# Optimization experiments

Measured on AMD Instinct MI355X. Metric: run time of the kernel, lower is better.

Reference implementation:

```python
import jax, jax.numpy as jnp
import numpy as np

EMBED_DIM = 1024
HEADS = 16
HEAD_DIM = EMBED_DIM // HEADS


def setup_inputs() -> dict:
    key = jax.random.key(0)
    ks = jax.random.split(key, 5)
    B, N, C = 2, 2048, EMBED_DIM
    scale = 1.0 / np.sqrt(C)
    x = jax.random.normal(ks[0], (B, N, C), dtype=jnp.float32)
    W_qkv = jax.random.normal(ks[1], (C, 3 * C), dtype=jnp.float32) * scale
    b_qkv = jax.random.normal(ks[2], (3 * C,), dtype=jnp.float32) * 0.01
    W_out = jax.random.normal(ks[3], (C, C), dtype=jnp.float32) * scale
    b_out = jax.random.normal(ks[4], (C,), dtype=jnp.float32) * 0.01
    return {"x": x, "W_qkv": W_qkv, "b_qkv": b_qkv, "W_out": W_out, "b_out": b_out}


def reference(x, W_qkv, b_qkv, W_out, b_out):
    B, N, C = x.shape
    qkv = x @ W_qkv + b_qkv                      # [B, N, 3C]
    qkv = qkv.reshape(B, N, 3, HEADS, HEAD_DIM)
    qkv = jnp.transpose(qkv, (2, 0, 3, 1, 4))    # [3, B, H, N, d]
    q, k, v = qkv[0], qkv[1], qkv[2]
    attn = jnp.einsum('bhnd,bhmd->bhnm', q, k) / np.sqrt(HEAD_DIM)
    attn = jax.nn.softmax(attn, axis=-1)
    out = jnp.einsum('bhnm,bhmd->bhnd', attn, v)  # [B, H, N, d]
    out = jnp.transpose(out, (0, 2, 1, 3)).reshape(B, N, C)
    return out @ W_out + b_out
```

## Files before the change

kernel.cpp:

```cpp
#include <hip/hip_runtime.h>
#include <stdint.h>

typedef __bf16 bf16_t;
typedef bf16_t bf16x8 __attribute__((ext_vector_type(8)));
typedef bf16_t bf16x2v __attribute__((ext_vector_type(2)));
typedef short short4v __attribute__((ext_vector_type(4)));
typedef float f32x4 __attribute__((ext_vector_type(4)));
typedef uint32_t u32x2 __attribute__((ext_vector_type(2)));

#define BATCH 2
#define SEQ 2048
#define CDIM 1024
#define NH 16
#define HD 64

#define QSCALE 0.18033688011f

__device__ __forceinline__ uint16_t f32_bf16(float f) {
    __bf16 h = (__bf16)f;
    return __builtin_bit_cast(uint16_t, h);
}

__device__ __forceinline__ uint32_t pack_bf16(float a, float b) {
    bf16x2v t;
    t.x = (__bf16)a;
    t.y = (__bf16)b;
    return __builtin_bit_cast(uint32_t, t);
}

__device__ __forceinline__ bf16x8 ld8(const uint16_t* p) {
    return *reinterpret_cast<const bf16x8*>(p);
}

__device__ __forceinline__ void gld16(const uint16_t* g, uint16_t* l) {
    __builtin_amdgcn_global_load_lds(
        (__attribute__((address_space(1))) void*)(g),
        (__attribute__((address_space(3))) void*)(l), 16, 0, 0);
}

#define LDS_FENCE() asm volatile("s_waitcnt lgkmcnt(0)" ::: "memory")

__global__ __launch_bounds__(256) void cast_f32_bf16(
        const float* __restrict__ in, uint16_t* __restrict__ out, int n) {
    int i = (blockIdx.x * 256 + threadIdx.x) * 4;
    if (i < n) {
        float4 v = *(const float4*)(in + i);
        ushort4 o;
        o.x = f32_bf16(v.x);
        o.y = f32_bf16(v.y);
        o.z = f32_bf16(v.z);
        o.w = f32_bf16(v.w);
        *(ushort4*)(out + i) = o;
    }
}

__global__ __launch_bounds__(256) void transpose_cast(
        const float* __restrict__ in, uint16_t* __restrict__ out, int R, int Cc) {
    __shared__ float tile[32][33];
    int c0 = blockIdx.x * 32, r0 = blockIdx.y * 32;
    int tx = threadIdx.x, ty = threadIdx.y;
#pragma unroll
    for (int i = 0; i < 4; i++) {
        int r = ty + i * 8;
        tile[r][tx] = in[(size_t)(r0 + r) * Cc + c0 + tx];
    }
    __syncthreads();
#pragma unroll
    for (int i = 0; i < 4; i++) {
        int rr = ty + i * 8;
        out[(size_t)(c0 + rr) * R + r0 + tx] = f32_bf16(tile[tx][rr]);
    }
}

__global__ __launch_bounds__(256) void gemm128(
        const uint16_t* __restrict__ A, const uint16_t* __restrict__ Bt, int K,
        const float* __restrict__ bias, int mode,
        uint16_t* __restrict__ qw, uint16_t* __restrict__ kw, uint16_t* __restrict__ vt,
        float* __restrict__ out) {
    __shared__ uint16_t As[128 * 32];
    __shared__ uint16_t Bs[128 * 32];
    __shared__ uint16_t Ts[4][64 * 68];
    const int m0 = blockIdx.y * 128, n0 = blockIdx.x * 128;
    const int tid = threadIdx.x;
    const int w = tid >> 6, lane = tid & 63;
    const int quad = lane >> 4, l16 = lane & 15;
    const int wm = (w >> 1) * 64, wn = (w & 1) * 64;

    const int srow = lane >> 2;
    const int schunk = (lane & 3) ^ (srow & 3);
    const int seg0 = w * 2, seg1 = seg0 + 1;
    const uint16_t* a0 = A + (size_t)(m0 + seg0 * 16 + srow) * K + schunk * 8;
    const uint16_t* a1 = A + (size_t)(m0 + seg1 * 16 + srow) * K + schunk * 8;
    const uint16_t* b0 = Bt + (size_t)(n0 + seg0 * 16 + srow) * K + schunk * 8;
    const uint16_t* b1 = Bt + (size_t)(n0 + seg1 * 16 + srow) * K + schunk * 8;
    uint16_t* la0 = &As[seg0 * 512];
    uint16_t* la1 = &As[seg1 * 512];
    uint16_t* lb0 = &Bs[seg0 * 512];
    uint16_t* lb1 = &Bs[seg1 * 512];

    const int cslot = (quad ^ (l16 & 3)) * 8;

    f32x4 acc[4][4] = {};

    for (int k0 = 0; k0 < K; k0 += 32) {
        gld16(a0 + k0, la0);
        gld16(a1 + k0, la1);
        gld16(b0 + k0, lb0);
        gld16(b1 + k0, lb1);
        __syncthreads();
        bf16x8 af[4], bfr[4];
#pragma unroll
        for (int i = 0; i < 4; i++) af[i] = ld8(&As[(wm + i * 16 + l16) * 32 + cslot]);
#pragma unroll
        for (int i = 0; i < 4; i++) bfr[i] = ld8(&Bs[(wn + i * 16 + l16) * 32 + cslot]);
#pragma unroll
        for (int i = 0; i < 4; i++)
#pragma unroll
            for (int j = 0; j < 4; j++)
                acc[i][j] = __builtin_amdgcn_mfma_f32_16x16x32_bf16(af[i], bfr[j], acc[i][j], 0, 0, 0);
        __syncthreads();
    }

    const int nbase = n0 + wn;
    float bj[4];
#pragma unroll
    for (int j = 0; j < 4; j++) bj[j] = bias[nbase + j * 16 + l16];

    if (mode == 1) {
#pragma unroll
        for (int j = 0; j < 4; j++) {
#pragma unroll
            for (int i = 0; i < 4; i++)
#pragma unroll
                for (int r = 0; r < 4; r++) {
                    int m = m0 + wm + i * 16 + quad * 4 + r;
                    out[(size_t)m * CDIM + nbase + j * 16 + l16] = acc[i][j][r] + bj[j];
                }
        }
        return;
    }

    uint16_t* T = &Ts[w][0];
    const int gmb = m0 + wm;
    const int b = gmb >> 11, ns0 = gmb & 2047;

    if (nbase < 2048) {
        const int which = nbase >> 10, h = (nbase & 1023) >> 6;
        const float sc = (which == 0) ? QSCALE : 1.0f;
#pragma unroll
        for (int i = 0; i < 4; i++)
#pragma unroll
            for (int j = 0; j < 4; j++)
#pragma unroll
                for (int r = 0; r < 4; r++)
                    T[(i * 16 + quad * 4 + r) * 68 + j * 16 + l16] =
                        f32_bf16((acc[i][j][r] + bj[j]) * sc);
        LDS_FENCE();
        uint16_t* dst = ((which == 0) ? qw : kw) +
                        (((size_t)b * NH + h) * SEQ + ns0 + lane) * HD;
#pragma unroll
        for (int g = 0; g < 8; g++) {
            bf16x8 v = ld8(&T[lane * 68 + g * 8]);
            *(bf16x8*)(dst + g * 8) = v;
        }
    } else {
#pragma unroll
        for (int i = 0; i < 4; i++)
#pragma unroll
            for (int j = 0; j < 4; j++) {
                u32x2 pr;
                pr.x = pack_bf16(acc[i][j][0] + bj[j], acc[i][j][1] + bj[j]);
                pr.y = pack_bf16(acc[i][j][2] + bj[j], acc[i][j][3] + bj[j]);
                *(u32x2*)&T[(j * 16 + l16) * 68 + i * 16 + quad * 4] = pr;
            }
        LDS_FENCE();
        const int h = (nbase - 2048) >> 6;
        uint16_t* dst = vt + (((size_t)b * NH + h) * HD + lane) * SEQ + ns0;
#pragma unroll
        for (int g = 0; g < 16; g++) {
            u32x2 d2 = *(const u32x2*)&T[lane * 68 + g * 4];
            int npos = (g & 3) * 16 + (g >> 2) * 4;
            *(u32x2*)(dst + npos) = d2;
        }
    }
}

__global__ __launch_bounds__(256) void attn_kernel(
        const uint16_t* __restrict__ qg, const uint16_t* __restrict__ kg,
        const uint16_t* __restrict__ vt, uint16_t* __restrict__ og) {
    __shared__ uint16_t Ks[2][64 * 64];
    __shared__ uint16_t Vs[2][64 * 64];

    const int bh = blockIdx.x;
    const int qt = blockIdx.y;
    const int tid = threadIdx.x;
    const int w = tid >> 6, lane = tid & 63;
    const int quad = lane >> 4, l16 = lane & 15;
    const int qrow0 = qt * 64 + w * 16;
    const size_t base = (size_t)bh * SEQ * HD;

    bf16x8 qf[2];
#pragma unroll
    for (int ks = 0; ks < 2; ks++)
        qf[ks] = ld8(qg + base + (size_t)(qrow0 + l16) * HD + ks * 32 + quad * 8);

    const int srow = lane >> 3;
    const int schunk = (lane & 7) ^ srow;
    const int seg0 = w * 2, seg1 = seg0 + 1;
    const uint16_t* ksrc0 = kg + base + (size_t)(seg0 * 8 + srow) * HD + schunk * 8;
    const uint16_t* ksrc1 = kg + base + (size_t)(seg1 * 8 + srow) * HD + schunk * 8;
    const uint16_t* vsrc0 = vt + base + (size_t)(seg0 * 8 + srow) * SEQ + schunk * 8;
    const uint16_t* vsrc1 = vt + base + (size_t)(seg1 * 8 + srow) * SEQ + schunk * 8;
    const int soff0 = seg0 * 512, soff1 = seg1 * 512;

    f32x4 o_acc[4] = {};
    f32x4 l_acc = {};
    const short4v ones = { (short)0x3F80, (short)0x3F80, (short)0x3F80, (short)0x3F80 };

    gld16(ksrc0, &Ks[0][soff0]); gld16(ksrc1, &Ks[0][soff1]);
    gld16(vsrc0, &Vs[0][soff0]); gld16(vsrc1, &Vs[0][soff1]);
    ksrc0 += 64 * HD; ksrc1 += 64 * HD; vsrc0 += 64; vsrc1 += 64;

    for (int it = 0; it < SEQ / 64; ++it) {
        __syncthreads();
        if (it + 1 < SEQ / 64) {
            int pb = (it + 1) & 1;
            gld16(ksrc0, &Ks[pb][soff0]); gld16(ksrc1, &Ks[pb][soff1]);
            gld16(vsrc0, &Vs[pb][soff0]); gld16(vsrc1, &Vs[pb][soff1]);
            ksrc0 += 64 * HD; ksrc1 += 64 * HD; vsrc0 += 64; vsrc1 += 64;
        }
        const uint16_t* K_ = Ks[it & 1];
        const uint16_t* V_ = Vs[it & 1];

        f32x4 S[4] = {};
#pragma unroll
        for (int nf = 0; nf < 4; nf++) {
#pragma unroll
            for (int ks = 0; ks < 2; ks++) {
                bf16x8 kf = ld8(&K_[(nf * 16 + l16) * 64 + (((ks * 4 + quad) ^ (l16 & 7)) * 8)]);
                S[nf] = __builtin_amdgcn_mfma_f32_16x16x32_bf16(kf, qf[ks], S[nf], 0, 0, 0);
            }
        }

        uint32_t pk[4][2];
#pragma unroll
        for (int nf = 0; nf < 4; nf++) {
            float p0 = __builtin_amdgcn_exp2f(S[nf][0]);
            float p1 = __builtin_amdgcn_exp2f(S[nf][1]);
            float p2 = __builtin_amdgcn_exp2f(S[nf][2]);
            float p3 = __builtin_amdgcn_exp2f(S[nf][3]);
            pk[nf][0] = pack_bf16(p0, p1);
            pk[nf][1] = pack_bf16(p2, p3);
        }

#pragma unroll
        for (int kc = 0; kc < 4; kc++) {
            short4v pfrag = __builtin_bit_cast(short4v, (u32x2){pk[kc][0], pk[kc][1]});
            l_acc = __builtin_amdgcn_mfma_f32_16x16x16bf16_1k(ones, pfrag, l_acc, 0, 0, 0);
        }

#pragma unroll
        for (int mf = 0; mf < 4; mf++) {
            const int ro = (mf * 16 + l16) * 64;
            uint4 v0 = *(const uint4*)&V_[ro + (((quad * 2 + 0) ^ (l16 & 7)) * 8)];
            uint4 v1 = *(const uint4*)&V_[ro + (((quad * 2 + 1) ^ (l16 & 7)) * 8)];
            short4v vf[4];
            vf[0] = __builtin_bit_cast(short4v, (u32x2){v0.x, v0.y});
            vf[1] = __builtin_bit_cast(short4v, (u32x2){v0.z, v0.w});
            vf[2] = __builtin_bit_cast(short4v, (u32x2){v1.x, v1.y});
            vf[3] = __builtin_bit_cast(short4v, (u32x2){v1.z, v1.w});
#pragma unroll
            for (int kc = 0; kc < 4; kc++) {
                short4v pfrag = __builtin_bit_cast(short4v, (u32x2){pk[kc][0], pk[kc][1]});
                o_acc[mf] = __builtin_amdgcn_mfma_f32_16x16x16bf16_1k(vf[kc], pfrag, o_acc[mf], 0, 0, 0);
            }
        }
    }

    const int b = bh >> 4, h = bh & 15;
    const float inv = __builtin_amdgcn_rcpf(l_acc[0]);
    const int ns = qrow0 + l16;
    uint16_t* orow = og + (((size_t)b * SEQ + ns) * NH + h) * HD + quad * 4;
#pragma unroll
    for (int mf = 0; mf < 4; mf++) {
        ushort4 o;
        o.x = f32_bf16(o_acc[mf][0] * inv);
        o.y = f32_bf16(o_acc[mf][1] * inv);
        o.z = f32_bf16(o_acc[mf][2] * inv);
        o.w = f32_bf16(o_acc[mf][3] * inv);
        *(ushort4*)(orow + mf * 16) = o;
    }
}

extern "C" void kernel_launch(void* const* d_in, const int* in_sizes, int n_in,
                              void* d_out, int out_size, void* d_ws, size_t ws_size,
                              hipStream_t stream) {
    const float* x = (const float*)d_in[0];
    const float* Wqkv = (const float*)d_in[1];
    const float* bqkv = (const float*)d_in[2];
    const float* Wout = (const float*)d_in[3];
    const float* bout = (const float*)d_in[4];
    float* out = (float*)d_out;

    uint16_t* ws = (uint16_t*)d_ws;
    uint16_t* x_bf  = ws;
    uint16_t* wqkvT = x_bf + 4194304;
    uint16_t* woutT = wqkvT + 3145728;
    uint16_t* qw    = woutT + 1048576;
    uint16_t* kw    = qw + 4194304;
    uint16_t* vtw   = kw + 4194304;
    uint16_t* attn  = vtw + 4194304;

    cast_f32_bf16<<<4096, 256, 0, stream>>>(x, x_bf, 4194304);
    transpose_cast<<<dim3(96, 32), dim3(32, 8), 0, stream>>>(Wqkv, wqkvT, 1024, 3072);
    transpose_cast<<<dim3(32, 32), dim3(32, 8), 0, stream>>>(Wout, woutT, 1024, 1024);

    gemm128<<<dim3(24, 32), 256, 0, stream>>>(x_bf, wqkvT, 1024, bqkv, 0, qw, kw, vtw, nullptr);

    attn_kernel<<<dim3(32, 32), 256, 0, stream>>>(qw, kw, vtw, attn);

    gemm128<<<dim3(8, 32), 256, 0, stream>>>(attn, woutT, 1024, bout, 1, nullptr, nullptr, nullptr, out);
}
```

Before: 210.5 us.

## Merge prep kernels, double-buffer GEMM LDS, retile output projection

Folds the x cast and both weight transpose-casts into one launch, which removes two kernel launches. The GEMM becomes a template that double-buffers its LDS tiles, so the next K-slice loads while MFMAs run and the second barrier per iteration goes away. The output projection switches to 64x128 tiles to double its block count (256 to 512) and fill more CUs. The costs are a larger LDS footprint per block and an extra barrier before the epilogue reuses shared memory.

```diff
diff --git a/kernel.cpp b/kernel.cpp
--- a/kernel.cpp
+++ b/kernel.cpp
@@ -40,147 +40,173 @@
 
 #define LDS_FENCE() asm volatile("s_waitcnt lgkmcnt(0)" ::: "memory")
 
-__global__ __launch_bounds__(256) void cast_f32_bf16(
-        const float* __restrict__ in, uint16_t* __restrict__ out, int n) {
-    int i = (blockIdx.x * 256 + threadIdx.x) * 4;
-    if (i < n) {
-        float4 v = *(const float4*)(in + i);
+__global__ __launch_bounds__(256) void prep_kernel(
+        const float* __restrict__ x, uint16_t* __restrict__ x_bf,
+        const float* __restrict__ Wqkv, uint16_t* __restrict__ wqkvT,
+        const float* __restrict__ Wout, uint16_t* __restrict__ woutT) {
+    const int bid = blockIdx.x, tid = threadIdx.x;
+    if (bid < 4096) {
+        int i = (bid * 256 + tid) * 4;
+        float4 v = *(const float4*)(x + i);
         ushort4 o;
         o.x = f32_bf16(v.x);
         o.y = f32_bf16(v.y);
         o.z = f32_bf16(v.z);
         o.w = f32_bf16(v.w);
-        *(ushort4*)(out + i) = o;
-    }
-}
-
-__global__ __launch_bounds__(256) void transpose_cast(
-        const float* __restrict__ in, uint16_t* __restrict__ out, int R, int Cc) {
+        *(ushort4*)(x_bf + i) = o;
+        return;
+    }
     __shared__ float tile[32][33];
-    int c0 = blockIdx.x * 32, r0 = blockIdx.y * 32;
-    int tx = threadIdx.x, ty = threadIdx.y;
-#pragma unroll
-    for (int i = 0; i < 4; i++) {
-        int r = ty + i * 8;
-        tile[r][tx] = in[(size_t)(r0 + r) * Cc + c0 + tx];
-    }
+    const float* in;
+    uint16_t* outp;
+    int idx, Cc, ncx;
+    if (bid < 4096 + 3072) { idx = bid - 4096; in = Wqkv; outp = wqkvT; Cc = 3072; ncx = 96; }
+    else                   { idx = bid - 7168; in = Wout; outp = woutT; Cc = 1024; ncx = 32; }
+    const int R = 1024;
+    int bx = idx % ncx, by = idx / ncx;
+    int c0 = bx * 32, r0 = by * 32;
+    int tx = tid & 31, ty = tid >> 5;
+#pragma unroll
+    for (int i = 0; i < 4; i++)
+        tile[ty + i * 8][tx] = in[(size_t)(r0 + ty + i * 8) * Cc + c0 + tx];
     __syncthreads();
 #pragma unroll
     for (int i = 0; i < 4; i++) {
         int rr = ty + i * 8;
-        out[(size_t)(c0 + rr) * R + r0 + tx] = f32_bf16(tile[tx][rr]);
-    }
-}
-
-__global__ __launch_bounds__(256) void gemm128(
+        outp[(size_t)(c0 + rr) * R + r0 + tx] = f32_bf16(tile[tx][rr]);
+    }
+}
+
+template <int BM, int BN, int MODE>
+__global__ __launch_bounds__(256) void gemm_t(
         const uint16_t* __restrict__ A, const uint16_t* __restrict__ Bt, int K,
-        const float* __restrict__ bias, int mode,
+        const float* __restrict__ bias,
         uint16_t* __restrict__ qw, uint16_t* __restrict__ kw, uint16_t* __restrict__ vt,
         float* __restrict__ out) {
-    __shared__ uint16_t As[128 * 32];
-    __shared__ uint16_t Bs[128 * 32];
-    __shared__ uint16_t Ts[4][64 * 68];
-    const int m0 = blockIdx.y * 128, n0 = blockIdx.x * 128;
+    constexpr int WT_M = BM / 2, WT_N = BN / 2;
+    constexpr int MI = WT_M / 16, NJ = WT_N / 16;
+    constexpr int ASEG_W = BM / 64, BSEG_W = BN / 64;
+    constexpr int AB = 2 * BM * 32 + 2 * BN * 32;
+    constexpr int TS = (MODE == 0) ? 4 * 64 * 68 : 0;
+    constexpr int SM = AB > TS ? AB : TS;
+    __shared__ uint16_t smem[SM];
+    uint16_t* As = smem;
+    uint16_t* Bs = smem + 2 * BM * 32;
+
+    const int m0 = blockIdx.y * BM, n0 = blockIdx.x * BN;
     const int tid = threadIdx.x;
     const int w = tid >> 6, lane = tid & 63;
     const int quad = lane >> 4, l16 = lane & 15;
-    const int wm = (w >> 1) * 64, wn = (w & 1) * 64;
+    const int wm = (w >> 1) * WT_M, wn = (w & 1) * WT_N;
 
     const int srow = lane >> 2;
     const int schunk = (lane & 3) ^ (srow & 3);
-    const int seg0 = w * 2, seg1 = seg0 + 1;
-    const uint16_t* a0 = A + (size_t)(m0 + seg0 * 16 + srow) * K + schunk * 8;
-    const uint16_t* a1 = A + (size_t)(m0 + seg1 * 16 + srow) * K + schunk * 8;
-    const uint16_t* b0 = Bt + (size_t)(n0 + seg0 * 16 + srow) * K + schunk * 8;
-    const uint16_t* b1 = Bt + (size_t)(n0 + seg1 * 16 + srow) * K + schunk * 8;
-    uint16_t* la0 = &As[seg0 * 512];
-    uint16_t* la1 = &As[seg1 * 512];
-    uint16_t* lb0 = &Bs[seg0 * 512];
-    uint16_t* lb1 = &Bs[seg1 * 512];
+
+    const uint16_t* aP[ASEG_W];
+    const uint16_t* bP[BSEG_W];
+    int aL[ASEG_W], bL[BSEG_W];
+#pragma unroll
+    for (int s = 0; s < ASEG_W; s++) {
+        int seg = w * ASEG_W + s;
+        aP[s] = A + (size_t)(m0 + seg * 16 + srow) * K + schunk * 8;
+        aL[s] = seg * 512;
+    }
+#pragma unroll
+    for (int s = 0; s < BSEG_W; s++) {
+        int seg = w * BSEG_W + s;
+        bP[s] = Bt + (size_t)(n0 + seg * 16 + srow) * K + schunk * 8;
+        bL[s] = seg * 512;
+    }
+
+    auto stage = [&](int buf, int k0) {
+#pragma unroll
+        for (int s = 0; s < ASEG_W; s++) gld16(aP[s] + k0, As + buf * BM * 32 + aL[s]);
+#pragma unroll
+        for (int s = 0; s < BSEG_W; s++) gld16(bP[s] + k0, Bs + buf * BN * 32 + bL[s]);
+    };
 
     const int cslot = (quad ^ (l16 & 3)) * 8;
-
-    f32x4 acc[4][4] = {};
-
-    for (int k0 = 0; k0 < K; k0 += 32) {
-        gld16(a0 + k0, la0);
-        gld16(a1 + k0, la1);
-        gld16(b0 + k0, lb0);
-        gld16(b1 + k0, lb1);
+    f32x4 acc[MI][NJ] = {};
+
+    stage(0, 0);
+    const int iters = K / 32;
+    for (int it = 0; it < iters; ++it) {
         __syncthreads();
-        bf16x8 af[4], bfr[4];
-#pragma unroll
-        for (int i = 0; i < 4; i++) af[i] = ld8(&As[(wm + i * 16 + l16) * 32 + cslot]);
-#pragma unroll
-        for (int i = 0; i < 4; i++) bfr[i] = ld8(&Bs[(wn + i * 16 + l16) * 32 + cslot]);
-#pragma unroll
-        for (int i = 0; i < 4; i++)
-#pragma unroll
-            for (int j = 0; j < 4; j++)
+        if (it + 1 < iters) stage((it + 1) & 1, (it + 1) * 32);
+        const uint16_t* A_ = As + (it & 1) * BM * 32;
+        const uint16_t* B_ = Bs + (it & 1) * BN * 32;
+        bf16x8 af[MI], bfr[NJ];
+#pragma unroll
+        for (int i = 0; i < MI; i++) af[i] = ld8(&A_[(wm + i * 16 + l16) * 32 + cslot]);
+#pragma unroll
+        for (int j = 0; j < NJ; j++) bfr[j] = ld8(&B_[(wn + j * 16 + l16) * 32 + cslot]);
+#pragma unroll
+        for (int i = 0; i < MI; i++)
+#pragma unroll
+            for (int j = 0; j < NJ; j++)
                 acc[i][j] = __builtin_amdgcn_mfma_f32_16x16x32_bf16(af[i], bfr[j], acc[i][j], 0, 0, 0);
-        __syncthreads();
     }
 
     const int nbase = n0 + wn;
-    float bj[4];
-#pragma unroll
-    for (int j = 0; j < 4; j++) bj[j] = bias[nbase + j * 16 + l16];
-
-    if (mode == 1) {
-#pragma unroll
-        for (int j = 0; j < 4; j++) {
-#pragma unroll
-            for (int i = 0; i < 4; i++)
+    float bj[NJ];
+#pragma unroll
+    for (int j = 0; j < NJ; j++) bj[j] = bias[nbase + j * 16 + l16];
+
+    if constexpr (MODE == 1) {
+#pragma unroll
+        for (int j = 0; j < NJ; j++) {
+#pragma unroll
+            for (int i = 0; i < MI; i++)
 #pragma unroll
                 for (int r = 0; r < 4; r++) {
                     int m = m0 + wm + i * 16 + quad * 4 + r;
                     out[(size_t)m * CDIM + nbase + j * 16 + l16] = acc[i][j][r] + bj[j];
                 }
         }
-        return;
-    }
-
-    uint16_t* T = &Ts[w][0];
-    const int gmb = m0 + wm;
-    const int b = gmb >> 11, ns0 = gmb & 2047;
-
-    if (nbase < 2048) {
-        const int which = nbase >> 10, h = (nbase & 1023) >> 6;
-        const float sc = (which == 0) ? QSCALE : 1.0f;
-#pragma unroll
-        for (int i = 0; i < 4; i++)
-#pragma unroll
-            for (int j = 0; j < 4; j++)
-#pragma unroll
-                for (int r = 0; r < 4; r++)
-                    T[(i * 16 + quad * 4 + r) * 68 + j * 16 + l16] =
-                        f32_bf16((acc[i][j][r] + bj[j]) * sc);
-        LDS_FENCE();
-        uint16_t* dst = ((which == 0) ? qw : kw) +
-                        (((size_t)b * NH + h) * SEQ + ns0 + lane) * HD;
-#pragma unroll
-        for (int g = 0; g < 8; g++) {
-            bf16x8 v = ld8(&T[lane * 68 + g * 8]);
-            *(bf16x8*)(dst + g * 8) = v;
-        }
     } else {
-#pragma unroll
-        for (int i = 0; i < 4; i++)
-#pragma unroll
-            for (int j = 0; j < 4; j++) {
-                u32x2 pr;
-                pr.x = pack_bf16(acc[i][j][0] + bj[j], acc[i][j][1] + bj[j]);
-                pr.y = pack_bf16(acc[i][j][2] + bj[j], acc[i][j][3] + bj[j]);
-                *(u32x2*)&T[(j * 16 + l16) * 68 + i * 16 + quad * 4] = pr;
+        __syncthreads();
+        uint16_t* T = smem + w * 64 * 68;
+        const int gmb = m0 + wm;
+        const int b = gmb >> 11, ns0 = gmb & 2047;
+
+        if (nbase < 2048) {
+            const int which = nbase >> 10, h = (nbase & 1023) >> 6;
+            const float sc = (which == 0) ? QSCALE : 1.0f;
+#pragma unroll
+            for (int i = 0; i < 4; i++)
+#pragma unroll
+                for (int j = 0; j < 4; j++)
+#pragma unroll
+                    for (int r = 0; r < 4; r++)
+                        T[(i * 16 + quad * 4 + r) * 68 + j * 16 + l16] =
+                            f32_bf16((acc[i][j][r] + bj[j]) * sc);
+            LDS_FENCE();
+            uint16_t* dst = ((which == 0) ? qw : kw) +
+                            (((size_t)b * NH + h) * SEQ + ns0 + lane) * HD;
+#pragma unroll
+            for (int g = 0; g < 8; g++) {
+                bf16x8 v = ld8(&T[lane * 68 + g * 8]);
+                *(bf16x8*)(dst + g * 8) = v;
             }
-        LDS_FENCE();
-        const int h = (nbase - 2048) >> 6;
-        uint16_t* dst = vt + (((size_t)b * NH + h) * HD + lane) * SEQ + ns0;
-#pragma unroll
-        for (int g = 0; g < 16; g++) {
-            u32x2 d2 = *(const u32x2*)&T[lane * 68 + g * 4];
-            int npos = (g & 3) * 16 + (g >> 2) * 4;
-            *(u32x2*)(dst + npos) = d2;
+        } else {
+#pragma unroll
+            for (int i = 0; i < 4; i++)
+#pragma unroll
+                for (int j = 0; j < 4; j++) {
+                    u32x2 pr;
+                    pr.x = pack_bf16(acc[i][j][0] + bj[j], acc[i][j][1] + bj[j]);
+                    pr.y = pack_bf16(acc[i][j][2] + bj[j], acc[i][j][3] + bj[j]);
+                    *(u32x2*)&T[(j * 16 + l16) * 68 + i * 16 + quad * 4] = pr;
+                }
+            LDS_FENCE();
+            const int h = (nbase - 2048) >> 6;
+            uint16_t* dst = vt + (((size_t)b * NH + h) * HD + lane) * SEQ + ns0;
+#pragma unroll
+            for (int g = 0; g < 16; g++) {
+                u32x2 d2 = *(const u32x2*)&T[lane * 68 + g * 4];
+                int npos = (g & 3) * 16 + (g >> 2) * 4;
+                *(u32x2*)(dst + npos) = d2;
+            }
         }
     }
 }
@@ -311,13 +337,13 @@
     uint16_t* vtw   = kw + 4194304;
     uint16_t* attn  = vtw + 4194304;
 
-    cast_f32_bf16<<<4096, 256, 0, stream>>>(x, x_bf, 4194304);
-    transpose_cast<<<dim3(96, 32), dim3(32, 8), 0, stream>>>(Wqkv, wqkvT, 1024, 3072);
-    transpose_cast<<<dim3(32, 32), dim3(32, 8), 0, stream>>>(Wout, woutT, 1024, 1024);
-
-    gemm128<<<dim3(24, 32), 256, 0, stream>>>(x_bf, wqkvT, 1024, bqkv, 0, qw, kw, vtw, nullptr);
+    prep_kernel<<<8192, 256, 0, stream>>>(x, x_bf, Wqkv, wqkvT, Wout, woutT);
+
+    gemm_t<128, 128, 0><<<dim3(24, 32), 256, 0, stream>>>(
+        x_bf, wqkvT, 1024, bqkv, qw, kw, vtw, nullptr);
 
     attn_kernel<<<dim3(32, 32), 256, 0, stream>>>(qw, kw, vtw, attn);
 
-    gemm128<<<dim3(8, 32), 256, 0, stream>>>(attn, woutT, 1024, bout, 1, nullptr, nullptr, nullptr, out);
-}
+    gemm_t<64, 128, 1><<<dim3(8, 64), 256, 0, stream>>>(
+        attn, woutT, 1024, bout, nullptr, nullptr, nullptr, out);
+}
```

Result: faster. 192.1 us (-8.7%).
